# Performance work log

Hardware: AMD Instinct MI355X
Metric: run time of the kernel (lower is better)

## Reference

```python
import jax, jax.numpy as jnp
import numpy as np

SIZE = 4096      # number of 2D images stacked on channel axis
IMG = 64         # image_size
N_MULTS = 4      # len(mul_approx_func_arr)


def setup_inputs() -> dict:
    key = jax.random.key(0)
    k1, k2, k3 = jax.random.split(key, 3)
    inp = jax.random.normal(k1, (1, SIZE, IMG, IMG), dtype=jnp.float32)
    # Laplacian-sharpen init, tiled per multiplier index (as in __init__)
    base = jnp.asarray([-1., -1., -1., -1., 8., -1., -1., -1., -1.], dtype=jnp.float32) / 8.0
    weight = jnp.tile(base, (N_MULTS, 1)) + 0.01 * jax.random.normal(k2, (N_MULTS, 9), dtype=jnp.float32)
    weight_factor = jnp.full((N_MULTS, 1), 8.0, dtype=jnp.float32) + jax.random.normal(k3, (N_MULTS, 1), dtype=jnp.float32)
    return {"input": inp, "weight": weight, "weight_factor": weight_factor}


def reference(input, weight, weight_factor):
    # input: [1, C, H, W]; weight: [n, 9]; weight_factor: [n, 1]
    n = weight.shape[0]
    # hardtanh clamps (the in-place .data clamp makes these equivalent to clip)
    w = jnp.clip(weight, -1.0, 1.0) * jnp.clip(weight_factor, 1.0, 255.0)  # [n, 9]
    kernels = w.reshape(n, 1, 3, 3)

    # Unfold + per-element multiply + sum over the 9 taps == depthwise 3x3 conv
    # with the SAME kernel on every channel. Put channels on the batch axis so a
    # single conv evaluates all n mult indices at once. (mul_wrapper approximate
    # multiplier modeled as exact multiply.)
    x = input[0][:, None]  # [C, 1, H, W]
    conv = jax.lax.conv_general_dilated(
        x, kernels, window_strides=(1, 1), padding=((1, 1), (1, 1)),
        dimension_numbers=("NCHW", "OIHW", "NCHW"))  # [C, n, H, W]
    result = jnp.transpose(conv, (1, 0, 2, 3))[:, None]  # [n, 1, C, H, W]

    # approx_sharp: div = max(result)/128 per mult index; approx_division snaps
    # the divisor to the nearest power of two (round(log2(div))).
    div = jnp.max(result, axis=(1, 2, 3, 4), keepdims=True) / 128.0  # [n,1,1,1,1]
    shift = jnp.round(jnp.log2(div))
    shifted = result / jnp.exp2(shift)
    out = jnp.where(div > 0, shifted, result)
    # output[ii][0] = input + shifted result -> [n, 1, C, H, W]
    return input[None] + out
```

## Files before the change

kernel.cpp:

```cpp
#include <hip/hip_runtime.h>
#include <math.h>

#define NCH 4096
#define IMG 64
#define HW  (IMG * IMG)
#define NM  4

typedef float nfloat4 __attribute__((ext_vector_type(4)));

#define TP    69
#define TROWS 66
#define TILE_FLOATS (TROWS * TP)

#define GRID1 1024
#define CPB1  (NCH / GRID1)


__device__ __forceinline__ void load_weights(const float* __restrict__ wgt,
                                             const float* __restrict__ wf,
                                             float k[NM][9]) {
#pragma unroll
    for (int n = 0; n < NM; ++n) {
        float f = fminf(fmaxf(wf[n], 1.0f), 255.0f);
#pragma unroll
        for (int j = 0; j < 9; ++j) {
            float w = fminf(fmaxf(wgt[n * 9 + j], -1.0f), 1.0f);
            k[n][j] = w * f;
        }
    }
}

__device__ __forceinline__ void zero_border(float* tile, int t) {
#pragma unroll
    for (int b = t; b < 260; b += 256) {
        int r, cidx;
        if (b < 66)       { r = 0;            cidx = b; }
        else if (b < 132) { r = 65;           cidx = b - 66; }
        else if (b < 196) { r = b - 132 + 1;  cidx = 0; }
        else              { r = b - 196 + 1;  cidx = 65; }
        tile[r * TP + cidx] = 0.0f;
    }
}

__device__ __forceinline__ void stage_tile(const float* __restrict__ img,
                                           float* tile, int t) {
    const float4* img4 = (const float4*)img;
#pragma unroll
    for (int i = 0; i < 4; ++i) {
        int idx = t + i * 256;
        float4 v = img4[idx];
        int p = idx * 4;
        int h = p >> 6;
        int w = p & 63;
        float* dst = &tile[(h + 1) * TP + (w + 1)];
        dst[0] = v.x; dst[1] = v.y; dst[2] = v.z; dst[3] = v.w;
    }
}

__device__ __forceinline__ void load_taps(const float* tile, int h, int w0,
                                          float tap[3][6]) {
#pragma unroll
    for (int r = 0; r < 3; ++r) {
        const float* row = &tile[(h + r) * TP + w0];
#pragma unroll
        for (int cdx = 0; cdx < 6; ++cdx)
            tap[r][cdx] = row[cdx];
    }
}

__global__ __launch_bounds__(256) void conv_max_kernel(
        const float* __restrict__ in, const float* __restrict__ wgt,
        const float* __restrict__ wf, float* __restrict__ ws) {
    __shared__ float tile[TILE_FLOATS];
    __shared__ float red[4][NM];
    const int t = threadIdx.x;

    float k[NM][9];
    load_weights(wgt, wf, k);
    zero_border(tile, t);

    float m[NM] = {-INFINITY, -INFINITY, -INFINITY, -INFINITY};

#pragma unroll
    for (int cc = 0; cc < CPB1; ++cc) {
        const int c = blockIdx.x * CPB1 + cc;
        const float* img = in + (size_t)c * HW;
        __syncthreads();
        stage_tile(img, tile, t);
        __syncthreads();

#pragma unroll
        for (int g = 0; g < 4; ++g) {
            int pix = (t + g * 256) * 4;
            int h = pix >> 6;
            int w0 = pix & 63;
            float tap[3][6];
            load_taps(tile, h, w0, tap);
#pragma unroll
            for (int i = 0; i < 4; ++i) {
#pragma unroll
                for (int n = 0; n < NM; ++n) {
                    float acc = 0.0f;
#pragma unroll
                    for (int dy = 0; dy < 3; ++dy)
#pragma unroll
                        for (int dx = 0; dx < 3; ++dx)
                            acc = fmaf(k[n][dy * 3 + dx], tap[dy][dx + i], acc);
                    m[n] = fmaxf(m[n], acc);
                }
            }
        }
    }

#pragma unroll
    for (int off = 32; off >= 1; off >>= 1)
#pragma unroll
        for (int n = 0; n < NM; ++n)
            m[n] = fmaxf(m[n], __shfl_down(m[n], off, 64));

    const int wave = t >> 6, lane = t & 63;
    if (lane == 0)
#pragma unroll
        for (int n = 0; n < NM; ++n) red[wave][n] = m[n];
    __syncthreads();
    if (t == 0) {
        float4 v;
        v.x = fmaxf(fmaxf(red[0][0], red[1][0]), fmaxf(red[2][0], red[3][0]));
        v.y = fmaxf(fmaxf(red[0][1], red[1][1]), fmaxf(red[2][1], red[3][1]));
        v.z = fmaxf(fmaxf(red[0][2], red[1][2]), fmaxf(red[2][2], red[3][2]));
        v.w = fmaxf(fmaxf(red[0][3], red[1][3]), fmaxf(red[2][3], red[3][3]));
        *(float4*)(ws + (size_t)blockIdx.x * NM) = v;
    }
}

__global__ __launch_bounds__(256) void conv_out_kernel(
        const float* __restrict__ in, const float* __restrict__ wgt,
        const float* __restrict__ wf, const float* __restrict__ ws,
        float* __restrict__ out) {
    __shared__ float tile[TILE_FLOATS];
    __shared__ float red[4][NM];
    const int c = blockIdx.x;
    const int t = threadIdx.x;
    const float* img = in + (size_t)c * HW;

    const float4* p4 = (const float4*)ws;
    float4 mm = {-INFINITY, -INFINITY, -INFINITY, -INFINITY};
#pragma unroll
    for (int i = 0; i < GRID1 / 256; ++i) {
        float4 v = p4[t + i * 256];
        mm.x = fmaxf(mm.x, v.x); mm.y = fmaxf(mm.y, v.y);
        mm.z = fmaxf(mm.z, v.z); mm.w = fmaxf(mm.w, v.w);
    }
#pragma unroll
    for (int off = 32; off >= 1; off >>= 1) {
        mm.x = fmaxf(mm.x, __shfl_down(mm.x, off, 64));
        mm.y = fmaxf(mm.y, __shfl_down(mm.y, off, 64));
        mm.z = fmaxf(mm.z, __shfl_down(mm.z, off, 64));
        mm.w = fmaxf(mm.w, __shfl_down(mm.w, off, 64));
    }
    const int wave = t >> 6, lane = t & 63;
    if (lane == 0) {
        red[wave][0] = mm.x; red[wave][1] = mm.y;
        red[wave][2] = mm.z; red[wave][3] = mm.w;
    }
    __syncthreads();
    float fin[NM];
#pragma unroll
    for (int n = 0; n < NM; ++n)
        fin[n] = fmaxf(fmaxf(red[0][n], red[1][n]), fmaxf(red[2][n], red[3][n]));

    float inv[NM];
#pragma unroll
    for (int n = 0; n < NM; ++n) {
        float div = fin[n] * (1.0f / 128.0f);
        if (div > 0.0f) {
            float shift = rintf(log2f(div));
            inv[n] = exp2f(-shift);
        } else {
            inv[n] = 1.0f;
        }
    }

    float k[NM][9];
    load_weights(wgt, wf, k);

    __syncthreads();
    zero_border(tile, t);
    stage_tile(img, tile, t);
    __syncthreads();

#pragma unroll
    for (int g = 0; g < 4; ++g) {
        int pix = (t + g * 256) * 4;
        int h = pix >> 6;
        int w0 = pix & 63;
        float tap[3][6];
        load_taps(tile, h, w0, tap);
#pragma unroll
        for (int n = 0; n < NM; ++n) {
            nfloat4 o;
#pragma unroll
            for (int i = 0; i < 4; ++i) {
                float acc = 0.0f;
#pragma unroll
                for (int dy = 0; dy < 3; ++dy)
#pragma unroll
                    for (int dx = 0; dx < 3; ++dx)
                        acc = fmaf(k[n][dy * 3 + dx], tap[dy][dx + i], acc);
                o[i] = tap[1][i + 1] + acc * inv[n];
            }
            size_t off = ((size_t)n * NCH + c) * HW + pix;
            __builtin_nontemporal_store(o, (nfloat4*)(out + off));
        }
    }
}

extern "C" void kernel_launch(void* const* d_in, const int* in_sizes, int n_in,
                              void* d_out, int out_size, void* d_ws, size_t ws_size,
                              hipStream_t stream) {
    const float* in  = (const float*)d_in[0];
    const float* wgt = (const float*)d_in[1];
    const float* wf  = (const float*)d_in[2];
    float* out = (float*)d_out;
    float* ws  = (float*)d_ws;

    conv_max_kernel<<<dim3(GRID1), dim3(256), 0, stream>>>(in, wgt, wf, ws);
    conv_out_kernel<<<dim3(NCH), dim3(256), 0, stream>>>(in, wgt, wf, ws, out);
}
```

Measured before the change: 317.1 us.

## Double-buffer image tiles and prefetch next channel into registers

The max kernel now uses two shared-memory tiles and loads the next channel's image into registers while computing the current one, which cuts one barrier per channel and overlaps the global loads with compute. The output kernel issues its image load before the cross-block max reduction so the loads overlap that work. In exchange the max kernel uses twice the shared memory and more registers, which may lower occupancy.

```diff
diff --git a/kernel.cpp b/kernel.cpp
--- a/kernel.cpp
+++ b/kernel.cpp
@@ -42,18 +42,24 @@
     }
 }
 
-__device__ __forceinline__ void stage_tile(const float* __restrict__ img,
-                                           float* tile, int t) {
+__device__ __forceinline__ void load_img_regs(const float* __restrict__ img,
+                                              int t, float4 v[4]) {
     const float4* img4 = (const float4*)img;
+#pragma unroll
+    for (int i = 0; i < 4; ++i)
+        v[i] = img4[t + i * 256];
+}
+
+__device__ __forceinline__ void write_tile_regs(float* tile, int t,
+                                                const float4 v[4]) {
 #pragma unroll
     for (int i = 0; i < 4; ++i) {
         int idx = t + i * 256;
-        float4 v = img4[idx];
         int p = idx * 4;
         int h = p >> 6;
         int w = p & 63;
         float* dst = &tile[(h + 1) * TP + (w + 1)];
-        dst[0] = v.x; dst[1] = v.y; dst[2] = v.z; dst[3] = v.w;
+        dst[0] = v[i].x; dst[1] = v[i].y; dst[2] = v[i].z; dst[3] = v[i].w;
     }
 }
 
@@ -65,50 +71,61 @@
 #pragma unroll
         for (int cdx = 0; cdx < 6; ++cdx)
             tap[r][cdx] = row[cdx];
+    }
+}
+
+__device__ __forceinline__ void conv_max_tile(const float* tile, int t,
+                                              const float k[NM][9], float m[NM]) {
+#pragma unroll
+    for (int g = 0; g < 4; ++g) {
+        int pix = (t + g * 256) * 4;
+        int h = pix >> 6;
+        int w0 = pix & 63;
+        float tap[3][6];
+        load_taps(tile, h, w0, tap);
+#pragma unroll
+        for (int i = 0; i < 4; ++i) {
+#pragma unroll
+            for (int n = 0; n < NM; ++n) {
+                float acc = 0.0f;
+#pragma unroll
+                for (int dy = 0; dy < 3; ++dy)
+#pragma unroll
+                    for (int dx = 0; dx < 3; ++dx)
+                        acc = fmaf(k[n][dy * 3 + dx], tap[dy][dx + i], acc);
+                m[n] = fmaxf(m[n], acc);
+            }
+        }
     }
 }
 
 __global__ __launch_bounds__(256) void conv_max_kernel(
         const float* __restrict__ in, const float* __restrict__ wgt,
         const float* __restrict__ wf, float* __restrict__ ws) {
-    __shared__ float tile[TILE_FLOATS];
+    __shared__ float tile[2][TILE_FLOATS];
     __shared__ float red[4][NM];
     const int t = threadIdx.x;
-
+    const float* base = in + (size_t)blockIdx.x * CPB1 * HW;
+
+    float4 v[4];
+    load_img_regs(base, t, v);
     float k[NM][9];
     load_weights(wgt, wf, k);
-    zero_border(tile, t);
+    zero_border(tile[0], t);
+    zero_border(tile[1], t);
+    write_tile_regs(tile[0], t, v);
+    __syncthreads();
 
     float m[NM] = {-INFINITY, -INFINITY, -INFINITY, -INFINITY};
 
 #pragma unroll
     for (int cc = 0; cc < CPB1; ++cc) {
-        const int c = blockIdx.x * CPB1 + cc;
-        const float* img = in + (size_t)c * HW;
-        __syncthreads();
-        stage_tile(img, tile, t);
-        __syncthreads();
-
-#pragma unroll
-        for (int g = 0; g < 4; ++g) {
-            int pix = (t + g * 256) * 4;
-            int h = pix >> 6;
-            int w0 = pix & 63;
-            float tap[3][6];
-            load_taps(tile, h, w0, tap);
-#pragma unroll
-            for (int i = 0; i < 4; ++i) {
-#pragma unroll
-                for (int n = 0; n < NM; ++n) {
-                    float acc = 0.0f;
-#pragma unroll
-                    for (int dy = 0; dy < 3; ++dy)
-#pragma unroll
-                        for (int dx = 0; dx < 3; ++dx)
-                            acc = fmaf(k[n][dy * 3 + dx], tap[dy][dx + i], acc);
-                    m[n] = fmaxf(m[n], acc);
-                }
-            }
+        if (cc + 1 < CPB1)
+            load_img_regs(base + (size_t)(cc + 1) * HW, t, v);
+        conv_max_tile(tile[cc & 1], t, k, m);
+        if (cc + 1 < CPB1) {
+            write_tile_regs(tile[(cc + 1) & 1], t, v);
+            __syncthreads();
         }
     }
 
@@ -119,17 +136,18 @@
             m[n] = fmaxf(m[n], __shfl_down(m[n], off, 64));
 
     const int wave = t >> 6, lane = t & 63;
+    __syncthreads();
     if (lane == 0)
 #pragma unroll
         for (int n = 0; n < NM; ++n) red[wave][n] = m[n];
     __syncthreads();
     if (t == 0) {
-        float4 v;
-        v.x = fmaxf(fmaxf(red[0][0], red[1][0]), fmaxf(red[2][0], red[3][0]));
-        v.y = fmaxf(fmaxf(red[0][1], red[1][1]), fmaxf(red[2][1], red[3][1]));
-        v.z = fmaxf(fmaxf(red[0][2], red[1][2]), fmaxf(red[2][2], red[3][2]));
-        v.w = fmaxf(fmaxf(red[0][3], red[1][3]), fmaxf(red[2][3], red[3][3]));
-        *(float4*)(ws + (size_t)blockIdx.x * NM) = v;
+        float4 o;
+        o.x = fmaxf(fmaxf(red[0][0], red[1][0]), fmaxf(red[2][0], red[3][0]));
+        o.y = fmaxf(fmaxf(red[0][1], red[1][1]), fmaxf(red[2][1], red[3][1]));
+        o.z = fmaxf(fmaxf(red[0][2], red[1][2]), fmaxf(red[2][2], red[3][2]));
+        o.w = fmaxf(fmaxf(red[0][3], red[1][3]), fmaxf(red[2][3], red[3][3]));
+        *(float4*)(ws + (size_t)blockIdx.x * NM) = o;
     }
 }
 
@@ -143,13 +161,16 @@
     const int t = threadIdx.x;
     const float* img = in + (size_t)c * HW;
 
+    float4 v[4];
+    load_img_regs(img, t, v);
+
     const float4* p4 = (const float4*)ws;
     float4 mm = {-INFINITY, -INFINITY, -INFINITY, -INFINITY};
 #pragma unroll
     for (int i = 0; i < GRID1 / 256; ++i) {
-        float4 v = p4[t + i * 256];
-        mm.x = fmaxf(mm.x, v.x); mm.y = fmaxf(mm.y, v.y);
-        mm.z = fmaxf(mm.z, v.z); mm.w = fmaxf(mm.w, v.w);
+        float4 pv = p4[t + i * 256];
+        mm.x = fmaxf(mm.x, pv.x); mm.y = fmaxf(mm.y, pv.y);
+        mm.z = fmaxf(mm.z, pv.z); mm.w = fmaxf(mm.w, pv.w);
     }
 #pragma unroll
     for (int off = 32; off >= 1; off >>= 1) {
@@ -186,7 +207,7 @@
 
     __syncthreads();
     zero_border(tile, t);
-    stage_tile(img, tile, t);
+    write_tile_regs(tile, t, v);
     __syncthreads();
 
 #pragma unroll
```

Result: no change. 318.9 us (+0.6%).
